# Performance work log

Hardware: AMD Instinct MI355X
Metric: run time of the kernel (lower is better)

Reference implementation:

```python
import jax, jax.numpy as jnp
import numpy as np

B, Q, S, D, H = 4, 1024, 4096, 256, 8
HD = D // H
NEG = -1000000000.0


def setup_inputs() -> dict:
    key = jax.random.key(0)
    ks = jax.random.split(key, 12)
    s = 1.0 / np.sqrt(D)
    inp = {
        "query": jax.random.normal(ks[0], (B, Q, D), jnp.float32),
        "key": jax.random.normal(ks[1], (B, S, D), jnp.float32),
        "value": jax.random.normal(ks[2], (B, S, D), jnp.float32),
        "attention_mask": jax.random.randint(ks[3], (B, Q, S), 0, 2) > 0,
        # nn.Linear weights stored as [out, in]; we apply x @ W.T + b
        "wq": jax.random.uniform(ks[4], (D, D), jnp.float32, -s, s),
        "bq": jnp.zeros((D,), jnp.float32),
        "wk": jax.random.uniform(ks[5], (D, D), jnp.float32, -s, s),
        "bk": jnp.zeros((D,), jnp.float32),
        "wv": jax.random.uniform(ks[6], (D, D), jnp.float32, -s, s),
        "bv": jnp.zeros((D,), jnp.float32),
        "wo": jax.random.uniform(ks[7], (D, D), jnp.float32, -s, s),
        "bo": jnp.zeros((D,), jnp.float32),
        "ln_g": jnp.ones((D,), jnp.float32),
        "ln_b": jnp.zeros((D,), jnp.float32),
    }
    return inp


def _layernorm(x, g, b, eps=1e-5):
    mu = jnp.mean(x, axis=-1, keepdims=True)
    var = jnp.var(x, axis=-1, keepdims=True)
    return (x - mu) * jax.lax.rsqrt(var + eps) * g + b


def reference(query, key, value, attention_mask, wq, bq, wk, bk, wv, bv, wo, bo, ln_g, ln_b):
    residual = query
    x = _layernorm(query, ln_g, ln_b)
    q = x @ wq.T + bq                       # [B,Q,D]
    k = key @ wk.T + bk                     # [B,S,D]
    v = value @ wv.T + bv                   # [B,S,D]
    q = q.reshape(B, Q, H, HD).transpose(0, 2, 1, 3)   # [B,H,Q,HD]
    k = k.reshape(B, S, H, HD).transpose(0, 2, 1, 3)   # [B,H,S,HD]
    v = v.reshape(B, S, H, HD).transpose(0, 2, 1, 3)   # [B,H,S,HD]
    scale = HD ** -0.5
    scores = jnp.einsum("bhqd,bhsd->bhqs", q, k) * scale   # [B,H,Q,S]
    scores = jnp.where(attention_mask[:, None, :, :], scores, NEG)
    attn = jax.nn.softmax(scores, axis=-1)
    # dropout is identity in eval/inference mode
    out = jnp.einsum("bhqs,bhsd->bhqd", attn, v)            # [B,H,Q,HD]
    out = out.transpose(0, 2, 1, 3).reshape(B, Q, D)
    out = out @ wo.T + bo
    return out + residual
```

## Files before the change

### kernel.cpp

```cpp
#include <hip/hip_runtime.h>
#include <cmath>

#define BQ 4
#define QL 1024
#define SL 4096
#define DM 256
#define NH 8
#define HD 32
#define NROWS 32768
#define NSPLIT 4
#define SEG (SL / NSPLIT)

typedef __attribute__((ext_vector_type(8))) short short8;
typedef __attribute__((ext_vector_type(4))) short short4v;
typedef __attribute__((ext_vector_type(4))) float f32x4;
typedef __attribute__((ext_vector_type(4))) unsigned int uint4v;
typedef __attribute__((ext_vector_type(2))) unsigned int uint2v;
typedef unsigned long long u64;

#define MFMA16(a, b, c) __builtin_amdgcn_mfma_f32_16x16x32_bf16((a), (b), (c), 0, 0, 0)

__device__ __forceinline__ short f2bf(float f) {
  union { float f; unsigned int u; } x; x.f = f;
  unsigned int r = x.u + 0x7FFFu + ((x.u >> 16) & 1u);
  return (short)(r >> 16);
}
__device__ __forceinline__ unsigned int fu(float f) {
  union { float f; unsigned int u; } x; x.f = f; return x.u;
}
__device__ __forceinline__ unsigned int cvtpk(float lo, float hi) {
  unsigned int r;
  asm("v_cvt_pk_bf16_f32 %0, %1, %2" : "=v"(r) : "v"(lo), "v"(hi));
  return r;
}

__global__ __launch_bounds__(256) void wcvt_kernel(const float* __restrict__ wq,
                                                   const float* __restrict__ wk,
                                                   const float* __restrict__ wv,
                                                   const float* __restrict__ wo,
                                                   const uint4v* __restrict__ mask4,
                                                   unsigned int* __restrict__ flags,
                                                   short* __restrict__ w16) {
  if (blockIdx.x == 0) {
    __shared__ int fA, fB;
    if (threadIdx.x == 0) { fA = 0; fB = 0; }
    __syncthreads();
    unsigned int a = 0, bb = 0;
#pragma unroll
    for (int i = 0; i < 16; ++i) {
      uint4v v = mask4[threadIdx.x * 16 + i];
#pragma unroll
      for (int e = 0; e < 4; ++e) {
        a |= (v[e] & 0xFEFEFEFEu);
        bb |= (v[e] & 0xFFFFFF00u);
      }
    }
    if (a) atomicOr(&fA, 1);
    if (bb) atomicOr(&fB, 1);
    __syncthreads();
    if (threadIdx.x == 0) flags[0] = (fA || !fB) ? 4u : 1u;
  }
  const int i = blockIdx.x * 256 + threadIdx.x;
  const float* src;
  short* dst;
  if (i < 8192)       { src = wq + i * 8;            dst = w16 + i * 8; }
  else if (i < 16384) { src = wk + (i - 8192) * 8;   dst = w16 + 65536 + (i - 8192) * 8; }
  else if (i < 24576) { src = wv + (i - 16384) * 8;  dst = w16 + 131072 + (i - 16384) * 8; }
  else                { src = wo + (i - 24576) * 8;  dst = w16 + 196608 + (i - 24576) * 8; }
  f32x4 a0 = *(const f32x4*)src;
  f32x4 a1 = *(const f32x4*)(src + 4);
  uint4v o = {cvtpk(a0[0], a0[1]), cvtpk(a0[2], a0[3]),
              cvtpk(a1[0], a1[1]), cvtpk(a1[2], a1[3])};
  *(uint4v*)dst = o;
}

__global__ __launch_bounds__(256) void masknln_kernel(const void* __restrict__ mask,
                                                      const unsigned int* __restrict__ flags,
                                                      u64* __restrict__ MB,
                                                      const float* __restrict__ x,
                                                      const float* __restrict__ gw,
                                                      const float* __restrict__ bw,
                                                      short* __restrict__ xout) {
  const int i = blockIdx.x * 256 + threadIdx.x;
  u64 bits = 0;
  if (flags[0] == 4u) {
    const uint4v* src = (const uint4v*)mask + (size_t)i * 16;
#pragma unroll
    for (int c = 0; c < 16; ++c) {
      uint4v v = src[c];
      unsigned int nib = 0;
#pragma unroll
      for (int e = 0; e < 4; ++e) nib |= (v[e] != 0u ? 1u : 0u) << e;
      bits |= (u64)nib << ((c & 3) * 16 + (c >> 2) * 4);
    }
  } else {
    const uint4v* src = (const uint4v*)mask + (size_t)i * 4;
#pragma unroll
    for (int c = 0; c < 4; ++c) {
      uint4v v = src[c];
#pragma unroll
      for (int e4 = 0; e4 < 4; ++e4) {
        const unsigned int u = v[e4];
        unsigned int nib = 0;
        nib |= (u & 0x000000FFu) ? 1u : 0u;
        nib |= (u & 0x0000FF00u) ? 2u : 0u;
        nib |= (u & 0x00FF0000u) ? 4u : 0u;
        nib |= (u & 0xFF000000u) ? 8u : 0u;
        bits |= (u64)nib << (e4 * 16 + c * 4);
      }
    }
  }
  MB[i] = bits;
  const int lane = threadIdx.x & 63;
  const int row = blockIdx.x * 4 + (threadIdx.x >> 6);
  const float* xr = x + (size_t)row * DM;
  f32x4 v = *(const f32x4*)(xr + lane * 4);
  float s = v[0] + v[1] + v[2] + v[3];
  float s2 = v[0]*v[0] + v[1]*v[1] + v[2]*v[2] + v[3]*v[3];
#pragma unroll
  for (int m = 1; m < 64; m <<= 1) { s += __shfl_xor(s, m); s2 += __shfl_xor(s2, m); }
  const float mu = s * (1.0f / DM);
  const float var = s2 * (1.0f / DM) - mu * mu;
  const float inv = rsqrtf(var + 1e-5f);
  f32x4 gv = *(const f32x4*)(gw + lane * 4);
  f32x4 bv = *(const f32x4*)(bw + lane * 4);
  float y0 = (v[0] - mu) * inv * gv[0] + bv[0];
  float y1 = (v[1] - mu) * inv * gv[1] + bv[1];
  float y2 = (v[2] - mu) * inv * gv[2] + bv[2];
  float y3 = (v[3] - mu) * inv * gv[3] + bv[3];
  uint2v o = {cvtpk(y0, y1), cvtpk(y2, y3)};
  *(uint2v*)(xout + (size_t)row * DM + lane * 4) = o;
}

template <int AF32, int EPI>
__global__ __launch_bounds__(256) void gemm_bt(const void* __restrict__ Ap,
                                               const short* __restrict__ W16,
                                               const float* __restrict__ bias,
                                               void* __restrict__ outp,
                                               const float* __restrict__ resid,
                                               float oscale) {
  __shared__ __align__(16) short As[64][72];
  __shared__ __align__(16) short Bs[64][72];
  const int t = threadIdx.x;
  const int lane = t & 63, w = t >> 6;
  const int wm = w >> 1, wn = w & 1;
  const int g = lane >> 4, lr = lane & 15, gsh = g * 4;
  const int bid = blockIdx.x;
  const int x = bid & 7, j = bid >> 3;
  const int mt8 = gridDim.x >> 5;
  const int m0 = (x * mt8 + (j >> 2)) * 64;
  const int n0 = (j & 3) * 64;
  const int row = (t * 2) >> 3, cc0 = (t * 2) & 7;
  f32x4 acc[2][2] = {};

  const float* Af = (const float*)Ap;
  const short* A16 = (const short*)Ap;
  f32x4 apf[2][2];
  short8 aps[2];
  short8 bn[2];
#pragma unroll
  for (int c = 0; c < 2; ++c) {
    if (AF32) {
      const float* s = Af + (size_t)(m0 + row) * DM + (cc0 + c) * 8;
      apf[c][0] = *(const f32x4*)s;
      apf[c][1] = *(const f32x4*)(s + 4);
    } else {
      aps[c] = *(const short8*)(A16 + (size_t)(m0 + row) * DM + (cc0 + c) * 8);
    }
    bn[c] = *(const short8*)(W16 + (size_t)(n0 + row) * DM + (cc0 + c) * 8);
  }
  for (int k0 = 0; k0 < DM; k0 += 64) {
    if (k0) __syncthreads();
#pragma unroll
    for (int c = 0; c < 2; ++c) {
      if (AF32) {
        uint4v sv = {cvtpk(apf[c][0][0], apf[c][0][1]), cvtpk(apf[c][0][2], apf[c][0][3]),
                     cvtpk(apf[c][1][0], apf[c][1][1]), cvtpk(apf[c][1][2], apf[c][1][3])};
        *(uint4v*)&As[row][(cc0 + c) * 8] = sv;
      } else {
        *(short8*)&As[row][(cc0 + c) * 8] = aps[c];
      }
      *(short8*)&Bs[row][(cc0 + c) * 8] = bn[c];
    }
    __syncthreads();
    if (k0 < DM - 64) {
#pragma unroll
      for (int c = 0; c < 2; ++c) {
        if (AF32) {
          const float* s = Af + (size_t)(m0 + row) * DM + k0 + 64 + (cc0 + c) * 8;
          apf[c][0] = *(const f32x4*)s;
          apf[c][1] = *(const f32x4*)(s + 4);
        } else {
          aps[c] = *(const short8*)(A16 + (size_t)(m0 + row) * DM + k0 + 64 + (cc0 + c) * 8);
        }
        bn[c] = *(const short8*)(W16 + (size_t)(n0 + row) * DM + k0 + 64 + (cc0 + c) * 8);
      }
    }
#pragma unroll
    for (int ks = 0; ks < 2; ++ks) {
      short8 af[2], bfr[2];
#pragma unroll
      for (int i = 0; i < 2; ++i) af[i] = *(const short8*)&As[wm * 32 + i * 16 + lr][ks * 32 + g * 8];
#pragma unroll
      for (int jj = 0; jj < 2; ++jj) bfr[jj] = *(const short8*)&Bs[wn * 32 + jj * 16 + lr][ks * 32 + g * 8];
#pragma unroll
      for (int i = 0; i < 2; ++i)
#pragma unroll
        for (int jj = 0; jj < 2; ++jj) acc[i][jj] = MFMA16(af[i], bfr[jj], acc[i][jj]);
    }
  }
  if (EPI == 2) {
#pragma unroll
    for (int i = 0; i < 2; ++i)
#pragma unroll
      for (int jj = 0; jj < 2; ++jj)
#pragma unroll
        for (int r = 0; r < 4; ++r) {
          const int rr = m0 + wm * 32 + i * 16 + gsh + r;
          const int col = n0 + wn * 32 + jj * 16 + lr;
          ((float*)outp)[(size_t)rr * DM + col] =
              acc[i][jj][r] + bias[col] + resid[(size_t)rr * DM + col];
        }
  } else if (EPI == 0 || EPI == 1) {
    __syncthreads();
#pragma unroll
    for (int i = 0; i < 2; ++i)
#pragma unroll
      for (int jj = 0; jj < 2; ++jj) {
        const int nl = wn * 32 + jj * 16 + lr;
        const float bv = bias[n0 + nl];
#pragma unroll
        for (int r = 0; r < 4; ++r)
          As[wm * 32 + i * 16 + gsh + r][nl] = f2bf((acc[i][jj][r] + bv) * oscale);
      }
    __syncthreads();
#pragma unroll
    for (int c = 0; c < 2; ++c) {
      const int idx = t * 2 + c, dl = idx >> 3, ch = idx & 7;
      *(short8*)((short*)outp + (size_t)(m0 + dl) * DM + n0 + ch * 8) =
          *(const short8*)&As[dl][ch * 8];
    }
  } else {
    __syncthreads();
#pragma unroll
    for (int i = 0; i < 2; ++i)
#pragma unroll
      for (int jj = 0; jj < 2; ++jj) {
        const int nl = wn * 32 + jj * 16 + lr;
        const float bv = bias[n0 + nl];
        uint2v pk2 = {cvtpk(acc[i][jj][0] + bv, acc[i][jj][1] + bv),
                      cvtpk(acc[i][jj][2] + bv, acc[i][jj][3] + bv)};
        *(uint2v*)&As[nl][wm * 32 + i * 16 + gsh] = pk2;
      }
    __syncthreads();
    const int bidx = m0 >> 12, sbase = m0 & (SL - 1);
#pragma unroll
    for (int c = 0; c < 2; ++c) {
      const int idx = t * 2 + c, dl = idx >> 3, ch = idx & 7;
      *(short8*)((short*)outp + ((size_t)bidx * DM + n0 + dl) * SL + sbase + ch * 8) =
          *(const short8*)&As[dl][ch * 8];
    }
  }
}

__global__ __launch_bounds__(256, 4) void attn_kernel(const short* __restrict__ qb,
                                                      const short* __restrict__ kb,
                                                      const short* __restrict__ vbT,
                                                      const unsigned short* __restrict__ MB,
                                                      float* __restrict__ Op,
                                                      float* __restrict__ Lp) {
  __shared__ __align__(16) short Ks[2][64][40];
  __shared__ __align__(16) short Vs[2][32][76];

  const int n_ = blockIdx.x;
  const int x_ = n_ & 7, j_ = n_ >> 3;
  const int grp = ((j_ >> 5) << 3) + x_;
  const int within = j_ & 31;
  const int q0 = (within & 7) * 128;
  const int split = within >> 3;
  const int h = grp & 7, b = grp >> 3;

  const int t = threadIdx.x;
  const int l = t & 63, w = t >> 6;
  const int g = l >> 4, lr = l & 15, gsh = g * 4;
  const int qbase = q0 + w * 32;
  const int srow = t >> 2, scc = t & 3;
  const int vd = t >> 3, vsc = t & 7;

  const short* Kp = kb + ((size_t)b * SL + split * SEG + srow) * DM + h * HD + scc * 8;
  const short* Vp = vbT + ((size_t)(b * NH + h) * HD + vd) * SL + split * SEG + vsc * 8;
  const unsigned short* MBp0 =
      MB + (((size_t)(b * QL) + qbase + lr) * 64 + split * (SEG / 64)) * 4 + g;
  const unsigned short* MBp1 = MBp0 + 16 * 64 * 4;

  const short8 qf0 =
      *(const short8*)(qb + ((size_t)(b * QL) + qbase + lr) * DM + h * HD + g * 8);
  const short8 qf1 =
      *(const short8*)(qb + ((size_t)(b * QL) + qbase + 16 + lr) * DM + h * HD + g * 8);

  const short ONE = (short)0x3F80;
  const short8 ONES = {ONE, ONE, ONE, ONE, ONE, ONE, ONE, ONE};
  f32x4 Ov0[2] = {}, Ov1[2] = {};
  f32x4 Ls0 = {0.f, 0.f, 0.f, 0.f}, Ls1 = {0.f, 0.f, 0.f, 0.f};

  short8 kreg[2], vreg[2];
  unsigned int mbA[2], mbB[2];
  kreg[0] = *(const short8*)Kp;
  vreg[0] = *(const short8*)Vp;
  mbA[0] = MBp0[0]; mbB[0] = MBp1[0];
  kreg[1] = *(const short8*)(Kp + (size_t)64 * DM);
  vreg[1] = *(const short8*)(Vp + 64);
  mbA[1] = MBp0[4]; mbB[1] = MBp1[4];

#pragma unroll 2
  for (int it = 0; it < SEG / 64; ++it) {
    const int buf = it & 1;
    *(short8*)&Ks[buf][srow][scc * 8] = kreg[buf];
    {
      short4v lo = {vreg[buf][0], vreg[buf][1], vreg[buf][2], vreg[buf][3]};
      short4v hi = {vreg[buf][4], vreg[buf][5], vreg[buf][6], vreg[buf][7]};
      *(short4v*)&Vs[buf][vd][vsc * 8] = lo;
      *(short4v*)&Vs[buf][vd][vsc * 8 + 4] = hi;
    }
    const unsigned int mb0 = mbA[buf], mb1 = mbB[buf];
    __syncthreads();
    if (it < SEG / 64 - 2) {
      kreg[buf] = *(const short8*)(Kp + (size_t)(it + 2) * 64 * DM);
      vreg[buf] = *(const short8*)(Vp + (it + 2) * 64);
      mbA[buf] = MBp0[(it + 2) * 4];
      mbB[buf] = MBp1[(it + 2) * 4];
    }

    const f32x4 z = {0.f, 0.f, 0.f, 0.f};
    f32x4 sc0[4], sc1[4];
#pragma unroll
    for (int f = 0; f < 4; ++f) {
      short8 kf = *(const short8*)&Ks[buf][f * 16 + lr][g * 8];
      sc0[f] = MFMA16(kf, qf0, z);
      sc1[f] = MFMA16(kf, qf1, z);
    }
#pragma unroll
    for (int ks = 0; ks < 2; ++ks) {
      unsigned int pk0[2][2], pk1[2][2];
#pragma unroll
      for (int fi = 0; fi < 2; ++fi) {
        const int f = 2 * ks + fi;
        unsigned int p0[4], p1[4];
#pragma unroll
        for (int r = 0; r < 4; ++r) {
          const unsigned int m0b = (unsigned int)(-(int)((mb0 >> (f * 4 + r)) & 1u));
          const unsigned int m1b = (unsigned int)(-(int)((mb1 >> (f * 4 + r)) & 1u));
          p0[r] = fu(__builtin_amdgcn_exp2f(sc0[f][r])) & m0b;
          p1[r] = fu(__builtin_amdgcn_exp2f(sc1[f][r])) & m1b;
        }
        pk0[fi][0] = __builtin_amdgcn_perm(p0[0], p0[1], 0x03020706u);
        pk0[fi][1] = __builtin_amdgcn_perm(p0[2], p0[3], 0x03020706u);
        pk1[fi][0] = __builtin_amdgcn_perm(p1[0], p1[1], 0x03020706u);
        pk1[fi][1] = __builtin_amdgcn_perm(p1[2], p1[3], 0x03020706u);
      }
      union { unsigned int u[4]; short8 v; } pa0, pa1;
      pa0.u[0] = pk0[0][0]; pa0.u[1] = pk0[0][1]; pa0.u[2] = pk0[1][0]; pa0.u[3] = pk0[1][1];
      pa1.u[0] = pk1[0][0]; pa1.u[1] = pk1[0][1]; pa1.u[2] = pk1[1][0]; pa1.u[3] = pk1[1][1];
      Ls0 = MFMA16(pa0.v, ONES, Ls0);
      Ls1 = MFMA16(pa1.v, ONES, Ls1);
#pragma unroll
      for (int n = 0; n < 2; ++n) {
        short4v va = *(const short4v*)&Vs[buf][n * 16 + lr][(2 * ks) * 16 + gsh];
        short4v vb2 = *(const short4v*)&Vs[buf][n * 16 + lr][(2 * ks + 1) * 16 + gsh];
        union { short4v h[2]; short8 v; } vf;
        vf.h[0] = va; vf.h[1] = vb2;
        Ov0[n] = MFMA16(pa0.v, vf.v, Ov0[n]);
        Ov1[n] = MFMA16(pa1.v, vf.v, Ov1[n]);
      }
    }
  }
  const int ridx = (b * NH + h) * QL + qbase;
  const size_t pb = (size_t)split * NROWS + ridx;
#pragma unroll
  for (int n = 0; n < 2; ++n)
#pragma unroll
    for (int r = 0; r < 4; ++r) {
      Op[(pb + gsh + r) * 32 + n * 16 + lr] = Ov0[n][r];
      Op[(pb + 16 + gsh + r) * 32 + n * 16 + lr] = Ov1[n][r];
    }
  if (lr == 0) {
#pragma unroll
    for (int r = 0; r < 4; ++r) {
      Lp[pb + gsh + r] = Ls0[r];
      Lp[pb + 16 + gsh + r] = Ls1[r];
    }
  }
}

__global__ __launch_bounds__(256) void combine_kernel(const float* __restrict__ Op,
                                                      const float* __restrict__ Lp,
                                                      short* __restrict__ ao) {
  const int tid = blockIdx.x * 256 + threadIdx.x;
  const int r = tid >> 3;
  const int dq = (tid & 7) * 4;
  float den = 0.0f;
  f32x4 acc = {0.f, 0.f, 0.f, 0.f};
#pragma unroll
  for (int i = 0; i < NSPLIT; ++i) {
    den += Lp[(size_t)i * NROWS + r];
    const f32x4 o = *(const f32x4*)(Op + ((size_t)i * NROWS + r) * 32 + dq);
#pragma unroll
    for (int e = 0; e < 4; ++e) acc[e] += o[e];
  }
  const float inv = __builtin_amdgcn_rcpf(den);
  const int b = r >> 13, h = (r >> 10) & 7, q = r & 1023;
  uint2v o = {cvtpk(acc[0] * inv, acc[1] * inv), cvtpk(acc[2] * inv, acc[3] * inv)};
  *(uint2v*)(ao + ((size_t)(b * QL + q)) * DM + h * HD + dq) = o;
}

extern "C" void kernel_launch(void* const* d_in, const int* in_sizes, int n_in,
                              void* d_out, int out_size, void* d_ws, size_t ws_size,
                              hipStream_t stream) {
  const float* query = (const float*)d_in[0];
  const float* key   = (const float*)d_in[1];
  const float* value = (const float*)d_in[2];
  const void*  mask  = d_in[3];
  const float* wq = (const float*)d_in[4];
  const float* bq = (const float*)d_in[5];
  const float* wk = (const float*)d_in[6];
  const float* bk = (const float*)d_in[7];
  const float* wv = (const float*)d_in[8];
  const float* bv = (const float*)d_in[9];
  const float* wo = (const float*)d_in[10];
  const float* bo = (const float*)d_in[11];
  const float* lng = (const float*)d_in[12];
  const float* lnb = (const float*)d_in[13];
  float* out = (float*)d_out;

  char* ws = (char*)d_ws;
  unsigned int* flags = (unsigned int*)ws;
  float* Lp  = (float*)(ws + (4u << 10));
  short* xln = (short*)(ws + (2u << 20));
  short* qb  = (short*)(ws + (4u << 20));
  short* kb  = (short*)(ws + (6u << 20));
  short* vbT = (short*)(ws + (14u << 20));
  u64*   mbt = (u64*)(ws + (22u << 20));
  short* w16 = (short*)(ws + (24u << 20));
  float* Op  = (float*)(ws + (25u << 20));
  short* ao  = (short*)(ws + (41u << 20));

  const float qscale = (float)(1.4426950408889634 / sqrt((double)HD));

  wcvt_kernel<<<128, 256, 0, stream>>>(wq, wk, wv, wo, (const uint4v*)mask, flags, w16);
  masknln_kernel<<<1024, 256, 0, stream>>>(mask, flags, mbt, query, lng, lnb, xln);
  gemm_bt<0, 0><<<(BQ * QL / 64) * 4, 256, 0, stream>>>(xln, w16, bq, qb, nullptr, qscale);
  gemm_bt<1, 1><<<(BQ * SL / 64) * 4, 256, 0, stream>>>(key, w16 + 65536, bk, kb, nullptr, 1.0f);
  gemm_bt<1, 3><<<(BQ * SL / 64) * 4, 256, 0, stream>>>(value, w16 + 131072, bv, vbT, nullptr, 1.0f);
  attn_kernel<<<1024, 256, 0, stream>>>(qb, kb, vbT, (const unsigned short*)mbt, Op, Lp);
  combine_kernel<<<1024, 256, 0, stream>>>(Op, Lp, ao);
  gemm_bt<0, 2><<<(BQ * QL / 64) * 4, 256, 0, stream>>>(ao, w16 + 196608, bo, out, query, 1.0f);
}
```

Measured before the change: 92.70 us.

## Fuse split-softmax combine into output projection and add 32x32 GEMM tiles

Removes the separate combine kernel by having the output-projection GEMM read the partial attention outputs and denominators directly, normalise them and convert to bf16 while loading its A tile. The Q and output projections move to a new 32x32-tile GEMM with 1024 blocks to fill more CUs, and the GEMM loops use double-buffered shared memory so one barrier per k-step is dropped. This saves one launch and the intermediate ao write and read, at the cost of redundant partial-sum reads across the n-tiles of the output GEMM (each row's partials are reread by 8 column blocks).

```diff
diff --git a/kernel.cpp b/kernel.cpp
--- a/kernel.cpp
+++ b/kernel.cpp
@@ -132,15 +132,13 @@
   *(uint2v*)(xout + (size_t)row * DM + lane * 4) = o;
 }
 
-template <int AF32, int EPI>
-__global__ __launch_bounds__(256) void gemm_bt(const void* __restrict__ Ap,
+template <int EPI>
+__global__ __launch_bounds__(256) void gemm_bt(const float* __restrict__ Af,
                                                const short* __restrict__ W16,
                                                const float* __restrict__ bias,
-                                               void* __restrict__ outp,
-                                               const float* __restrict__ resid,
-                                               float oscale) {
-  __shared__ __align__(16) short As[64][72];
-  __shared__ __align__(16) short Bs[64][72];
+                                               void* __restrict__ outp) {
+  __shared__ __align__(16) short As[2][64][72];
+  __shared__ __align__(16) short Bs[2][64][72];
   const int t = threadIdx.x;
   const int lane = t & 63, w = t >> 6;
   const int wm = w >> 1, wn = w & 1;
@@ -153,76 +151,48 @@
   const int row = (t * 2) >> 3, cc0 = (t * 2) & 7;
   f32x4 acc[2][2] = {};
 
-  const float* Af = (const float*)Ap;
-  const short* A16 = (const short*)Ap;
   f32x4 apf[2][2];
-  short8 aps[2];
   short8 bn[2];
 #pragma unroll
   for (int c = 0; c < 2; ++c) {
-    if (AF32) {
-      const float* s = Af + (size_t)(m0 + row) * DM + (cc0 + c) * 8;
-      apf[c][0] = *(const f32x4*)s;
-      apf[c][1] = *(const f32x4*)(s + 4);
-    } else {
-      aps[c] = *(const short8*)(A16 + (size_t)(m0 + row) * DM + (cc0 + c) * 8);
-    }
+    const float* s = Af + (size_t)(m0 + row) * DM + (cc0 + c) * 8;
+    apf[c][0] = *(const f32x4*)s;
+    apf[c][1] = *(const f32x4*)(s + 4);
     bn[c] = *(const short8*)(W16 + (size_t)(n0 + row) * DM + (cc0 + c) * 8);
   }
-  for (int k0 = 0; k0 < DM; k0 += 64) {
-    if (k0) __syncthreads();
+  for (int k0 = 0; k0 < 4; ++k0) {
+    const int buf = k0 & 1;
 #pragma unroll
     for (int c = 0; c < 2; ++c) {
-      if (AF32) {
-        uint4v sv = {cvtpk(apf[c][0][0], apf[c][0][1]), cvtpk(apf[c][0][2], apf[c][0][3]),
-                     cvtpk(apf[c][1][0], apf[c][1][1]), cvtpk(apf[c][1][2], apf[c][1][3])};
-        *(uint4v*)&As[row][(cc0 + c) * 8] = sv;
-      } else {
-        *(short8*)&As[row][(cc0 + c) * 8] = aps[c];
-      }
-      *(short8*)&Bs[row][(cc0 + c) * 8] = bn[c];
-    }
-    __syncthreads();
-    if (k0 < DM - 64) {
+      uint4v sv = {cvtpk(apf[c][0][0], apf[c][0][1]), cvtpk(apf[c][0][2], apf[c][0][3]),
+                   cvtpk(apf[c][1][0], apf[c][1][1]), cvtpk(apf[c][1][2], apf[c][1][3])};
+      *(uint4v*)&As[buf][row][(cc0 + c) * 8] = sv;
+      *(short8*)&Bs[buf][row][(cc0 + c) * 8] = bn[c];
+    }
+    __syncthreads();
+    if (k0 < 3) {
 #pragma unroll
       for (int c = 0; c < 2; ++c) {
-        if (AF32) {
-          const float* s = Af + (size_t)(m0 + row) * DM + k0 + 64 + (cc0 + c) * 8;
-          apf[c][0] = *(const f32x4*)s;
-          apf[c][1] = *(const f32x4*)(s + 4);
-        } else {
-          aps[c] = *(const short8*)(A16 + (size_t)(m0 + row) * DM + k0 + 64 + (cc0 + c) * 8);
-        }
-        bn[c] = *(const short8*)(W16 + (size_t)(n0 + row) * DM + k0 + 64 + (cc0 + c) * 8);
+        const float* s = Af + (size_t)(m0 + row) * DM + (k0 + 1) * 64 + (cc0 + c) * 8;
+        apf[c][0] = *(const f32x4*)s;
+        apf[c][1] = *(const f32x4*)(s + 4);
+        bn[c] = *(const short8*)(W16 + (size_t)(n0 + row) * DM + (k0 + 1) * 64 + (cc0 + c) * 8);
       }
     }
 #pragma unroll
     for (int ks = 0; ks < 2; ++ks) {
       short8 af[2], bfr[2];
 #pragma unroll
-      for (int i = 0; i < 2; ++i) af[i] = *(const short8*)&As[wm * 32 + i * 16 + lr][ks * 32 + g * 8];
-#pragma unroll
-      for (int jj = 0; jj < 2; ++jj) bfr[jj] = *(const short8*)&Bs[wn * 32 + jj * 16 + lr][ks * 32 + g * 8];
+      for (int i = 0; i < 2; ++i) af[i] = *(const short8*)&As[buf][wm * 32 + i * 16 + lr][ks * 32 + g * 8];
+#pragma unroll
+      for (int jj = 0; jj < 2; ++jj) bfr[jj] = *(const short8*)&Bs[buf][wn * 32 + jj * 16 + lr][ks * 32 + g * 8];
 #pragma unroll
       for (int i = 0; i < 2; ++i)
 #pragma unroll
         for (int jj = 0; jj < 2; ++jj) acc[i][jj] = MFMA16(af[i], bfr[jj], acc[i][jj]);
     }
   }
-  if (EPI == 2) {
-#pragma unroll
-    for (int i = 0; i < 2; ++i)
-#pragma unroll
-      for (int jj = 0; jj < 2; ++jj)
-#pragma unroll
-        for (int r = 0; r < 4; ++r) {
-          const int rr = m0 + wm * 32 + i * 16 + gsh + r;
-          const int col = n0 + wn * 32 + jj * 16 + lr;
-          ((float*)outp)[(size_t)rr * DM + col] =
-              acc[i][jj][r] + bias[col] + resid[(size_t)rr * DM + col];
-        }
-  } else if (EPI == 0 || EPI == 1) {
-    __syncthreads();
+  if (EPI == 1) {
 #pragma unroll
     for (int i = 0; i < 2; ++i)
 #pragma unroll
@@ -231,17 +201,16 @@
         const float bv = bias[n0 + nl];
 #pragma unroll
         for (int r = 0; r < 4; ++r)
-          As[wm * 32 + i * 16 + gsh + r][nl] = f2bf((acc[i][jj][r] + bv) * oscale);
+          As[0][wm * 32 + i * 16 + gsh + r][nl] = f2bf(acc[i][jj][r] + bv);
       }
     __syncthreads();
 #pragma unroll
     for (int c = 0; c < 2; ++c) {
       const int idx = t * 2 + c, dl = idx >> 3, ch = idx & 7;
       *(short8*)((short*)outp + (size_t)(m0 + dl) * DM + n0 + ch * 8) =
-          *(const short8*)&As[dl][ch * 8];
+          *(const short8*)&As[0][dl][ch * 8];
     }
   } else {
-    __syncthreads();
 #pragma unroll
     for (int i = 0; i < 2; ++i)
 #pragma unroll
@@ -250,7 +219,7 @@
         const float bv = bias[n0 + nl];
         uint2v pk2 = {cvtpk(acc[i][jj][0] + bv, acc[i][jj][1] + bv),
                       cvtpk(acc[i][jj][2] + bv, acc[i][jj][3] + bv)};
-        *(uint2v*)&As[nl][wm * 32 + i * 16 + gsh] = pk2;
+        *(uint2v*)&As[0][nl][wm * 32 + i * 16 + gsh] = pk2;
       }
     __syncthreads();
     const int bidx = m0 >> 12, sbase = m0 & (SL - 1);
@@ -258,7 +227,96 @@
     for (int c = 0; c < 2; ++c) {
       const int idx = t * 2 + c, dl = idx >> 3, ch = idx & 7;
       *(short8*)((short*)outp + ((size_t)bidx * DM + n0 + dl) * SL + sbase + ch * 8) =
-          *(const short8*)&As[dl][ch * 8];
+          *(const short8*)&As[0][dl][ch * 8];
+    }
+  }
+}
+
+template <int EPI>
+__global__ __launch_bounds__(256) void gemm32(const short* __restrict__ A16,
+                                              const float* __restrict__ Op,
+                                              const float* __restrict__ Lp,
+                                              const short* __restrict__ W16,
+                                              const float* __restrict__ bias,
+                                              void* __restrict__ outp,
+                                              const float* __restrict__ resid,
+                                              float oscale) {
+  __shared__ __align__(16) short As[2][32][72];
+  __shared__ __align__(16) short Bs[2][32][72];
+  const int t = threadIdx.x;
+  const int lane = t & 63, w = t >> 6;
+  const int wm = w >> 1, wn = w & 1;
+  const int g = lane >> 4, lr = lane & 15, gsh = g * 4;
+  const int bid = blockIdx.x;
+  const int x = bid & 7, j = bid >> 3;
+  const int m0 = (x * 16 + (j >> 3)) * 32;
+  const int n0 = (j & 7) * 32;
+  const int row = t >> 3, cc = t & 7;
+  const int trow = m0 + row;
+  f32x4 acc = {0.f, 0.f, 0.f, 0.f};
+
+  short8 aval;
+  short8 bval;
+  auto produceA = [&](int k) -> short8 {
+    if (EPI == 0) {
+      return *(const short8*)(A16 + (size_t)trow * DM + k * 64 + cc * 8);
+    } else {
+      const int kcol = k * 64 + cc * 8;
+      const int h = kcol >> 5, hd = kcol & 31;
+      const size_t rid = ((size_t)((trow >> 10) * NH + h)) * QL + (trow & (QL - 1));
+      float den = 0.0f;
+      f32x4 o0 = {0.f, 0.f, 0.f, 0.f}, o1 = {0.f, 0.f, 0.f, 0.f};
+#pragma unroll
+      for (int i = 0; i < NSPLIT; ++i) {
+        const size_t base = ((size_t)i * NROWS + rid) * 32 + hd;
+        den += Lp[(size_t)i * NROWS + rid];
+        const f32x4 pa = *(const f32x4*)(Op + base);
+        const f32x4 pb = *(const f32x4*)(Op + base + 4);
+#pragma unroll
+        for (int e = 0; e < 4; ++e) { o0[e] += pa[e]; o1[e] += pb[e]; }
+      }
+      const float inv = __builtin_amdgcn_rcpf(den);
+      union { uint4v u; short8 s; } pk;
+      pk.u = uint4v{cvtpk(o0[0] * inv, o0[1] * inv), cvtpk(o0[2] * inv, o0[3] * inv),
+                    cvtpk(o1[0] * inv, o1[1] * inv), cvtpk(o1[2] * inv, o1[3] * inv)};
+      return pk.s;
+    }
+  };
+  aval = produceA(0);
+  bval = *(const short8*)(W16 + (size_t)(n0 + row) * DM + cc * 8);
+
+  for (int k0 = 0; k0 < 4; ++k0) {
+    const int buf = k0 & 1;
+    *(short8*)&As[buf][row][cc * 8] = aval;
+    *(short8*)&Bs[buf][row][cc * 8] = bval;
+    __syncthreads();
+    if (k0 < 3) {
+      aval = produceA(k0 + 1);
+      bval = *(const short8*)(W16 + (size_t)(n0 + row) * DM + (k0 + 1) * 64 + cc * 8);
+    }
+#pragma unroll
+    for (int ks = 0; ks < 2; ++ks) {
+      short8 af = *(const short8*)&As[buf][wm * 16 + lr][ks * 32 + g * 8];
+      short8 bf = *(const short8*)&Bs[buf][wn * 16 + lr][ks * 32 + g * 8];
+      acc = MFMA16(af, bf, acc);
+    }
+  }
+  if (EPI == 0) {
+    const int nl = wn * 16 + lr;
+    const float bv = bias[n0 + nl];
+#pragma unroll
+    for (int r = 0; r < 4; ++r)
+      As[0][wm * 16 + gsh + r][nl] = f2bf((acc[r] + bv) * oscale);
+    __syncthreads();
+    *(short4v*)((short*)outp + (size_t)trow * DM + n0 + (t & 7) * 4) =
+        *(const short4v*)&As[0][row][(t & 7) * 4];
+  } else {
+#pragma unroll
+    for (int r = 0; r < 4; ++r) {
+      const int rr = m0 + wm * 16 + gsh + r;
+      const int col = n0 + wn * 16 + lr;
+      ((float*)outp)[(size_t)rr * DM + col] =
+          acc[r] + bias[col] + resid[(size_t)rr * DM + col];
     }
   }
 }
@@ -390,27 +448,6 @@
       Lp[pb + 16 + gsh + r] = Ls1[r];
     }
   }
-}
-
-__global__ __launch_bounds__(256) void combine_kernel(const float* __restrict__ Op,
-                                                      const float* __restrict__ Lp,
-                                                      short* __restrict__ ao) {
-  const int tid = blockIdx.x * 256 + threadIdx.x;
-  const int r = tid >> 3;
-  const int dq = (tid & 7) * 4;
-  float den = 0.0f;
-  f32x4 acc = {0.f, 0.f, 0.f, 0.f};
-#pragma unroll
-  for (int i = 0; i < NSPLIT; ++i) {
-    den += Lp[(size_t)i * NROWS + r];
-    const f32x4 o = *(const f32x4*)(Op + ((size_t)i * NROWS + r) * 32 + dq);
-#pragma unroll
-    for (int e = 0; e < 4; ++e) acc[e] += o[e];
-  }
-  const float inv = __builtin_amdgcn_rcpf(den);
-  const int b = r >> 13, h = (r >> 10) & 7, q = r & 1023;
-  uint2v o = {cvtpk(acc[0] * inv, acc[1] * inv), cvtpk(acc[2] * inv, acc[3] * inv)};
-  *(uint2v*)(ao + ((size_t)(b * QL + q)) * DM + h * HD + dq) = o;
 }
 
 extern "C" void kernel_launch(void* const* d_in, const int* in_sizes, int n_in,
@@ -442,16 +479,14 @@
   u64*   mbt = (u64*)(ws + (22u << 20));
   short* w16 = (short*)(ws + (24u << 20));
   float* Op  = (float*)(ws + (25u << 20));
-  short* ao  = (short*)(ws + (41u << 20));
 
   const float qscale = (float)(1.4426950408889634 / sqrt((double)HD));
 
   wcvt_kernel<<<128, 256, 0, stream>>>(wq, wk, wv, wo, (const uint4v*)mask, flags, w16);
   masknln_kernel<<<1024, 256, 0, stream>>>(mask, flags, mbt, query, lng, lnb, xln);
-  gemm_bt<0, 0><<<(BQ * QL / 64) * 4, 256, 0, stream>>>(xln, w16, bq, qb, nullptr, qscale);
-  gemm_bt<1, 1><<<(BQ * SL / 64) * 4, 256, 0, stream>>>(key, w16 + 65536, bk, kb, nullptr, 1.0f);
-  gemm_bt<1, 3><<<(BQ * SL / 64) * 4, 256, 0, stream>>>(value, w16 + 131072, bv, vbT, nullptr, 1.0f);
+  gemm32<0><<<1024, 256, 0, stream>>>(xln, nullptr, nullptr, w16, bq, qb, nullptr, qscale);
+  gemm_bt<1><<<(BQ * SL / 64) * 4, 256, 0, stream>>>(key, w16 + 65536, bk, kb);
+  gemm_bt<3><<<(BQ * SL / 64) * 4, 256, 0, stream>>>(value, w16 + 131072, bv, vbT);
   attn_kernel<<<1024, 256, 0, stream>>>(qb, kb, vbT, (const unsigned short*)mbt, Op, Lp);
-  combine_kernel<<<1024, 256, 0, stream>>>(Op, Lp, ao);
-  gemm_bt<0, 2><<<(BQ * QL / 64) * 4, 256, 0, stream>>>(ao, w16 + 196608, bo, out, query, 1.0f);
-}
+  gemm32<2><<<1024, 256, 0, stream>>>(nullptr, Op, Lp, w16 + 196608, bo, out, query, 1.0f);
+}
```

Measured after the change: 92.29 us. Within noise of the previous version (-0.4%).
